# Kernel optimization log

Hardware: AMD Instinct MI355X
Metric: run time of the kernel (lower is better)

Reference implementation:

```python
import jax, jax.numpy as jnp
import numpy as np

T, N, F, H, E = 12, 10000, 32, 64, 320000


def setup_inputs() -> dict:
    key = jax.random.key(0)
    ks = jax.random.split(key, 6)
    x = jax.random.normal(ks[0], (T, N, F), dtype=jnp.float32)
    edge_index = jax.random.randint(ks[1], (2, E), 0, N, dtype=jnp.int64)
    edge_weight = jax.random.uniform(ks[2], (E,), dtype=jnp.float32)
    missing_mask = jnp.ones((T, N, F), dtype=jnp.bool_)
    # GCNConv params (Glorot-ish init); PyG lin: out = x @ W, bias added after aggregation
    W1 = jax.random.normal(ks[3], (F, H), dtype=jnp.float32) * (1.0 / np.sqrt(F))
    b1 = jnp.zeros((H,), dtype=jnp.float32)
    W2 = jax.random.normal(ks[4], (H, F), dtype=jnp.float32) * (1.0 / np.sqrt(H))
    b2 = jnp.zeros((F,), dtype=jnp.float32)
    return dict(x=x, edge_index=edge_index, edge_weight=edge_weight,
                missing_mask=missing_mask, W1=W1, b1=b1, W2=W2, b2=b2)


def _gcn_norm(edge_weight, row, col, n_nodes):
    # PyG gcn_norm with add_self_loops=False: deg from dst, sym normalization
    deg = jax.ops.segment_sum(edge_weight, col, num_segments=n_nodes)
    dinv = jnp.where(deg > 0, 1.0 / jnp.sqrt(jnp.maximum(deg, 1e-12)), 0.0)
    return dinv[row] * edge_weight * dinv[col]


def _gcn_layer(h, row, col, norm, W, b):
    # h: (T, N, Fin) -> (T, N, Fout). Gather at src, weight, scatter-add at dst.
    h = h @ W                                   # (T, N, Fout)
    msg = h[:, row, :] * norm[None, :, None]    # (T, E, Fout)
    out = jnp.zeros((h.shape[0], h.shape[1], h.shape[2]), h.dtype)
    out = out.at[:, col, :].add(msg)
    return out + b


def reference(x, edge_index, edge_weight, missing_mask, W1, b1, W2, b2):
    n_nodes = x.shape[1]
    row, col = edge_index[0], edge_index[1]
    norm = _gcn_norm(edge_weight, row, col, n_nodes)
    h = _gcn_layer(x, row, col, norm, W1, b1)   # layer 0
    h = jax.nn.relu(h)                          # relu between layers
    h = _gcn_layer(h, row, col, norm, W2, b2)   # layer 1 (out_dim = in_dim)
    return jnp.tanh(h)                          # original returns (x, 0); we return x
```

## Files before the change

### kernel.cpp

```cpp
#include <hip/hip_runtime.h>
#include <hip/hip_fp16.h>

#define T_DIM   12
#define N_NODES 10000
#define F_IN    32
#define H_DIM   64
#define NCH     3
#define TC      4
#define CHROW   (TC * F_IN)
#define NGRP    (N_NODES / 16)
#define NTASK   (NCH * NGRP)
#define NROWS   (NCH * N_NODES * TC)
#define MROWS   128

__global__ void zero_kernel(uint4* __restrict__ p, int n16) {
    int i = blockIdx.x * blockDim.x + threadIdx.x;
    if (i < n16) p[i] = make_uint4(0, 0, 0, 0);
}

__global__ void deg_hist_conv_kernel(const int* __restrict__ col,
                                     const float* __restrict__ w,
                                     float* __restrict__ deg,
                                     int* __restrict__ cnt, int E, int eb,
                                     const float* __restrict__ x,
                                     __half* __restrict__ xh) {
    int b = blockIdx.x;
    if (b < eb) {
        int e = b * 256 + threadIdx.x;
        if (e >= E) return;
        int c = col[e];
        atomicAdd(&deg[c], w[e]);
        atomicAdd(&cnt[c], 1);
    } else {
        int task = (b - eb) * 4 + (threadIdx.x >> 6);
        if (task >= NTASK) return;
        int l  = threadIdx.x & 63;
        int ch = task / NGRP;
        int ng = task - ch * NGRP;
        int n  = ng * 16 + (l >> 2);
        int t  = ch * TC + (l & 3);
        const float4* xp = (const float4*)(x + ((size_t)t * N_NODES + n) * F_IN);
        union { uint32_t u[16]; uint4 q[4]; } pk;
#pragma unroll
        for (int i = 0; i < 8; i++) {
            float4 v = xp[i];
            __half2 h0 = __floats2half2_rn(v.x, v.y);
            __half2 h1 = __floats2half2_rn(v.z, v.w);
            pk.u[2 * i]     = *(uint32_t*)&h0;
            pk.u[2 * i + 1] = *(uint32_t*)&h1;
        }
        uint4* dp = (uint4*)(xh + ((size_t)ch * N_NODES * TC + ng * 64 + l) * F_IN);
#pragma unroll
        for (int i = 0; i < 4; i++) dp[i] = pk.q[i];
    }
}

__global__ __launch_bounds__(1024) void scan_kernel(const int* __restrict__ cnt,
                                                    int* __restrict__ rowptr,
                                                    int* __restrict__ cur, int n) {
    __shared__ int part[1024];
    int tid = threadIdx.x;
    const int per = (n + 1023) / 1024;
    int base = tid * per;
    int s = 0;
    for (int i = 0; i < per; i++) {
        int idx = base + i;
        if (idx < n) s += cnt[idx];
    }
    part[tid] = s;
    __syncthreads();
    for (int off = 1; off < 1024; off <<= 1) {
        int v = 0;
        if (tid >= off) v = part[tid - off];
        __syncthreads();
        if (tid >= off) part[tid] += v;
        __syncthreads();
    }
    int run = (tid == 0) ? 0 : part[tid - 1];
    for (int i = 0; i < per; i++) {
        int idx = base + i;
        if (idx < n) { rowptr[idx] = run; cur[idx] = run; run += cnt[idx]; }
    }
    if (tid == 1023) rowptr[n] = part[1023];
}

__global__ void fill_kernel(const int* __restrict__ row,
                            const int* __restrict__ col,
                            const float* __restrict__ w,
                            const float* __restrict__ deg,
                            int* __restrict__ cur,
                            int2* __restrict__ edge_s, int E) {
    int e = blockIdx.x * blockDim.x + threadIdx.x;
    if (e >= E) return;
    int r = row[e];
    int c = col[e];
    float dr = deg[r];
    float dc = deg[c];
    float ir = dr > 0.f ? 1.0f / sqrtf(fmaxf(dr, 1e-12f)) : 0.f;
    float ic = dc > 0.f ? 1.0f / sqrtf(fmaxf(dc, 1e-12f)) : 0.f;
    float nw = ir * w[e] * ic;
    int pos = atomicAdd(&cur[c], 1);
    edge_s[pos] = make_int2(r, __float_as_int(nw));
}

template <bool TANH>
__global__ __launch_bounds__(256) void gather64_kernel(const int* __restrict__ rowptr,
                                                       const int2* __restrict__ edge_s,
                                                       const __half* __restrict__ yh,
                                                       const float* __restrict__ bias,
                                                       float* __restrict__ outp, int n) {
    int c = blockIdx.x * 4 + (threadIdx.x >> 6);
    if (c >= n) return;
    int l    = threadIdx.x & 63;
    int half = l >> 5;
    int l32  = l & 31;

    int beg = rowptr[c], end = rowptr[c + 1];
    const __half* base = yh + 4 * l32;
    const size_t cstep = (size_t)N_NODES * CHROW;

    float4 a0 = {0.f, 0.f, 0.f, 0.f};
    float4 a1 = {0.f, 0.f, 0.f, 0.f};
    float4 a2 = {0.f, 0.f, 0.f, 0.f};

#pragma unroll 4
    for (int e = beg + half; e < end; e += 2) {
        int2 ed = edge_s[e];
        float nw = __int_as_float(ed.y);
        const __half* p = base + (size_t)ed.x * CHROW;
        uint2 u0 = *(const uint2*)(p);
        uint2 u1 = *(const uint2*)(p + cstep);
        uint2 u2 = *(const uint2*)(p + 2 * cstep);
        float2 f00 = __half22float2(*(__half2*)&u0.x), f01 = __half22float2(*(__half2*)&u0.y);
        float2 f10 = __half22float2(*(__half2*)&u1.x), f11 = __half22float2(*(__half2*)&u1.y);
        float2 f20 = __half22float2(*(__half2*)&u2.x), f21 = __half22float2(*(__half2*)&u2.y);
        a0.x = fmaf(f00.x, nw, a0.x); a0.y = fmaf(f00.y, nw, a0.y);
        a0.z = fmaf(f01.x, nw, a0.z); a0.w = fmaf(f01.y, nw, a0.w);
        a1.x = fmaf(f10.x, nw, a1.x); a1.y = fmaf(f10.y, nw, a1.y);
        a1.z = fmaf(f11.x, nw, a1.z); a1.w = fmaf(f11.y, nw, a1.w);
        a2.x = fmaf(f20.x, nw, a2.x); a2.y = fmaf(f20.y, nw, a2.y);
        a2.z = fmaf(f21.x, nw, a2.z); a2.w = fmaf(f21.y, nw, a2.w);
    }

    a0.x += __shfl_xor(a0.x, 32); a0.y += __shfl_xor(a0.y, 32);
    a0.z += __shfl_xor(a0.z, 32); a0.w += __shfl_xor(a0.w, 32);
    a1.x += __shfl_xor(a1.x, 32); a1.y += __shfl_xor(a1.y, 32);
    a1.z += __shfl_xor(a1.z, 32); a1.w += __shfl_xor(a1.w, 32);
    a2.x += __shfl_xor(a2.x, 32); a2.y += __shfl_xor(a2.y, 32);
    a2.z += __shfl_xor(a2.z, 32); a2.w += __shfl_xor(a2.w, 32);

    if (TANH) {
        float4 b4 = *(const float4*)(bias + 4 * (l32 & 7));
        if (half == 0) {
            a0.x = tanhf(a0.x + b4.x); a0.y = tanhf(a0.y + b4.y);
            a0.z = tanhf(a0.z + b4.z); a0.w = tanhf(a0.w + b4.w);
            a1.x = tanhf(a1.x + b4.x); a1.y = tanhf(a1.y + b4.y);
            a1.z = tanhf(a1.z + b4.z); a1.w = tanhf(a1.w + b4.w);
            int t0 = (l32 >> 3);
            float* op0 = outp + ((size_t)t0 * N_NODES + c) * F_IN + 4 * (l32 & 7);
            *(float4*)(op0)                              = a0;
            *(float4*)(op0 + (size_t)TC * N_NODES * F_IN) = a1;
        } else {
            a2.x = tanhf(a2.x + b4.x); a2.y = tanhf(a2.y + b4.y);
            a2.z = tanhf(a2.z + b4.z); a2.w = tanhf(a2.w + b4.w);
            int t2 = 2 * TC + (l32 >> 3);
            float* op2 = outp + ((size_t)t2 * N_NODES + c) * F_IN + 4 * (l32 & 7);
            *(float4*)op2 = a2;
        }
    } else {
        float* op = outp + (size_t)c * CHROW + 4 * l32;
        const size_t ostep = (size_t)N_NODES * CHROW;
        if (half == 0) {
            *(float4*)(op)         = a0;
            *(float4*)(op + ostep) = a1;
        } else {
            *(float4*)(op + 2 * ostep) = a2;
        }
    }
}

__global__ __launch_bounds__(128) void mlp_kernel(const float* __restrict__ aggx,
                                                  const float* __restrict__ W1g,
                                                  const float* __restrict__ b1,
                                                  const float* __restrict__ W2g,
                                                  __half* __restrict__ y2h) {
    __shared__ float W1s[F_IN * H_DIM];
    __shared__ float W2s[H_DIM * F_IN];
    __shared__ float b1s[H_DIM];
    __shared__ float xs[MROWS][F_IN + 1];
    __shared__ float hs[MROWS][H_DIM + 1];

    int tid = threadIdx.x;
    for (int i = tid; i < F_IN * H_DIM; i += 128) { W1s[i] = W1g[i]; W2s[i] = W2g[i]; }
    if (tid < H_DIM) b1s[tid] = b1[tid];

    size_t row0 = (size_t)blockIdx.x * MROWS;
    const float4* src = (const float4*)(aggx + row0 * F_IN);
    for (int i = tid; i < MROWS * (F_IN / 4); i += 128) {
        float4 v = src[i];
        int r = i >> 3, q = (i & 7) * 4;
        xs[r][q + 0] = v.x; xs[r][q + 1] = v.y; xs[r][q + 2] = v.z; xs[r][q + 3] = v.w;
    }
    __syncthreads();

    int rg = tid >> 2;
    int cg = tid & 3;
    int r0 = 4 * rg;

    {
        int c0 = 16 * cg;
        float acc[4][16];
#pragma unroll
        for (int j = 0; j < 16; j++) {
            float b = b1s[c0 + j];
#pragma unroll
            for (int rr = 0; rr < 4; rr++) acc[rr][j] = b;
        }
#pragma unroll 8
        for (int k = 0; k < F_IN; k++) {
            float xr[4];
#pragma unroll
            for (int rr = 0; rr < 4; rr++) xr[rr] = xs[r0 + rr][k];
#pragma unroll
            for (int j = 0; j < 16; j++) {
                float wv = W1s[k * H_DIM + c0 + j];
#pragma unroll
                for (int rr = 0; rr < 4; rr++) acc[rr][j] = fmaf(xr[rr], wv, acc[rr][j]);
            }
        }
#pragma unroll
        for (int rr = 0; rr < 4; rr++)
#pragma unroll
            for (int j = 0; j < 16; j++)
                hs[r0 + rr][c0 + j] = fmaxf(acc[rr][j], 0.f);
    }
    __syncthreads();

    {
        int d0 = 8 * cg;
        float acc[4][8];
#pragma unroll
        for (int rr = 0; rr < 4; rr++)
#pragma unroll
            for (int j = 0; j < 8; j++) acc[rr][j] = 0.f;
#pragma unroll 8
        for (int k = 0; k < H_DIM; k++) {
            float hr[4];
#pragma unroll
            for (int rr = 0; rr < 4; rr++) hr[rr] = hs[r0 + rr][k];
#pragma unroll
            for (int j = 0; j < 8; j++) {
                float wv = W2s[k * F_IN + d0 + j];
#pragma unroll
                for (int rr = 0; rr < 4; rr++) acc[rr][j] = fmaf(hr[rr], wv, acc[rr][j]);
            }
        }
#pragma unroll
        for (int rr = 0; rr < 4; rr++) {
            union { uint32_t u[4]; uint4 q; } pk;
#pragma unroll
            for (int i = 0; i < 4; i++) {
                __half2 hh = __floats2half2_rn(acc[rr][2 * i], acc[rr][2 * i + 1]);
                pk.u[i] = *(uint32_t*)&hh;
            }
            *(uint4*)(y2h + (row0 + r0 + rr) * F_IN + d0) = pk.q;
        }
    }
}

extern "C" void kernel_launch(void* const* d_in, const int* in_sizes, int n_in,
                              void* d_out, int out_size, void* d_ws, size_t ws_size,
                              hipStream_t stream) {
    const float* x  = (const float*)d_in[0];
    const int*   ei = (const int*)d_in[1];
    const float* w  = (const float*)d_in[2];
    const float* W1 = (const float*)d_in[4];
    const float* b1 = (const float*)d_in[5];
    const float* W2 = (const float*)d_in[6];
    const float* b2 = (const float*)d_in[7];
    float* out = (float*)d_out;

    const int E = in_sizes[1] / 2;
    const int* row = ei;
    const int* col = ei + E;

    char* ws = (char*)d_ws;
    size_t off = 0;
    auto alloc = [&](size_t bytes) { void* p = ws + off; off += (bytes + 255) & ~(size_t)255; return p; };
    float*  deg    = (float*) alloc(N_NODES * sizeof(float));
    int*    cnt    = (int*)   alloc(N_NODES * sizeof(int));
    int*    cur    = (int*)   alloc(N_NODES * sizeof(int));
    int*    rowptr = (int*)   alloc((N_NODES + 1) * sizeof(int));
    int2*   edge_s = (int2*)  alloc((size_t)E * sizeof(int2));
    __half* xh     = (__half*)alloc((size_t)NROWS * F_IN * sizeof(__half));
    __half* y2h    = (__half*)alloc((size_t)(NROWS + 64) * F_IN * sizeof(__half));
    float*  aggx   = (float*) alloc((size_t)(NROWS + 64) * F_IN * sizeof(float));

    const int eb = (E + 255) / 256;
    const int cb = (NTASK + 3) / 4;
    const int gb = (N_NODES + 3) / 4;
    const int mb = (NROWS + MROWS - 1) / MROWS;

    const int zn = (int)(((char*)(cnt + N_NODES) - (char*)deg) / 16);
    zero_kernel<<<(zn + 255) / 256, 256, 0, stream>>>((uint4*)deg, zn);
    deg_hist_conv_kernel<<<eb + cb, 256, 0, stream>>>(col, w, deg, cnt, E, eb, x, xh);
    scan_kernel<<<1, 1024, 0, stream>>>(cnt, rowptr, cur, N_NODES);
    fill_kernel<<<eb, 256, 0, stream>>>(row, col, w, deg, cur, edge_s, E);

    gather64_kernel<false><<<gb, 256, 0, stream>>>(rowptr, edge_s, xh, nullptr, aggx, N_NODES);
    mlp_kernel<<<mb, 128, 0, stream>>>(aggx, W1, b1, W2, y2h);

    gather64_kernel<true><<<gb, 256, 0, stream>>>(rowptr, edge_s, y2h, b2, out, N_NODES);
}
```

Measured before the change: 165.8 us.

## Pack degree and count into one 64-bit atomic and precompute dinv

Replaces the separate float degree and int count atomics with a single 64-bit atomic holding a 20-bit fixed-point weight sum in the low bits and the edge count in the high bits. The returned old count gives each edge its slot within its destination, so the fill kernel no longer needs a second atomic on a cursor array. The scan kernel also computes rsqrt of each degree once, so fill reads dinv instead of doing per-edge sqrt and division. In exchange, the degree becomes fixed-point with limited precision and overflow headroom, and the extra per-edge posE buffer costs memory traffic.

Measured after the change: 137.1 us. -17.3%, faster.

```diff
diff --git a/kernel.cpp b/kernel.cpp
--- a/kernel.cpp
+++ b/kernel.cpp
@@ -13,6 +13,10 @@
 #define NROWS   (NCH * N_NODES * TC)
 #define MROWS   128
 
+#define CNT_SHIFT 40
+#define FIX_SCALE 1048576.0f
+#define FIX_MASK  ((1ull << CNT_SHIFT) - 1)
+
 __global__ void zero_kernel(uint4* __restrict__ p, int n16) {
     int i = blockIdx.x * blockDim.x + threadIdx.x;
     if (i < n16) p[i] = make_uint4(0, 0, 0, 0);
@@ -20,8 +24,8 @@
 
 __global__ void deg_hist_conv_kernel(const int* __restrict__ col,
                                      const float* __restrict__ w,
-                                     float* __restrict__ deg,
-                                     int* __restrict__ cnt, int E, int eb,
+                                     unsigned long long* __restrict__ packed,
+                                     unsigned int* __restrict__ posE, int E, int eb,
                                      const float* __restrict__ x,
                                      __half* __restrict__ xh) {
     int b = blockIdx.x;
@@ -29,8 +33,9 @@
         int e = b * 256 + threadIdx.x;
         if (e >= E) return;
         int c = col[e];
-        atomicAdd(&deg[c], w[e]);
-        atomicAdd(&cnt[c], 1);
+        unsigned long long fx = (unsigned long long)(w[e] * FIX_SCALE + 0.5f);
+        unsigned long long old = atomicAdd(&packed[c], (1ull << CNT_SHIFT) | fx);
+        posE[e] = (unsigned int)(old >> CNT_SHIFT);
     } else {
         int task = (b - eb) * 4 + (threadIdx.x >> 6);
         if (task >= NTASK) return;
@@ -55,9 +60,9 @@
     }
 }
 
-__global__ __launch_bounds__(1024) void scan_kernel(const int* __restrict__ cnt,
+__global__ __launch_bounds__(1024) void scan_kernel(const unsigned long long* __restrict__ packed,
                                                     int* __restrict__ rowptr,
-                                                    int* __restrict__ cur, int n) {
+                                                    float* __restrict__ dinv, int n) {
     __shared__ int part[1024];
     int tid = threadIdx.x;
     const int per = (n + 1023) / 1024;
@@ -65,7 +70,12 @@
     int s = 0;
     for (int i = 0; i < per; i++) {
         int idx = base + i;
-        if (idx < n) s += cnt[idx];
+        if (idx < n) {
+            unsigned long long p = packed[idx];
+            s += (int)(p >> CNT_SHIFT);
+            float deg = (float)(p & FIX_MASK) * (1.0f / FIX_SCALE);
+            dinv[idx] = deg > 0.f ? rsqrtf(deg) : 0.f;
+        }
     }
     part[tid] = s;
     __syncthreads();
@@ -79,7 +89,10 @@
     int run = (tid == 0) ? 0 : part[tid - 1];
     for (int i = 0; i < per; i++) {
         int idx = base + i;
-        if (idx < n) { rowptr[idx] = run; cur[idx] = run; run += cnt[idx]; }
+        if (idx < n) {
+            rowptr[idx] = run;
+            run += (int)(packed[idx] >> CNT_SHIFT);
+        }
     }
     if (tid == 1023) rowptr[n] = part[1023];
 }
@@ -87,19 +100,16 @@
 __global__ void fill_kernel(const int* __restrict__ row,
                             const int* __restrict__ col,
                             const float* __restrict__ w,
-                            const float* __restrict__ deg,
-                            int* __restrict__ cur,
+                            const float* __restrict__ dinv,
+                            const int* __restrict__ rowptr,
+                            const unsigned int* __restrict__ posE,
                             int2* __restrict__ edge_s, int E) {
     int e = blockIdx.x * blockDim.x + threadIdx.x;
     if (e >= E) return;
     int r = row[e];
     int c = col[e];
-    float dr = deg[r];
-    float dc = deg[c];
-    float ir = dr > 0.f ? 1.0f / sqrtf(fmaxf(dr, 1e-12f)) : 0.f;
-    float ic = dc > 0.f ? 1.0f / sqrtf(fmaxf(dc, 1e-12f)) : 0.f;
-    float nw = ir * w[e] * ic;
-    int pos = atomicAdd(&cur[c], 1);
+    float nw = dinv[r] * w[e] * dinv[c];
+    int pos = rowptr[c] + (int)posE[e];
     edge_s[pos] = make_int2(r, __float_as_int(nw));
 }
 
@@ -158,7 +168,7 @@
             a1.z = tanhf(a1.z + b4.z); a1.w = tanhf(a1.w + b4.w);
             int t0 = (l32 >> 3);
             float* op0 = outp + ((size_t)t0 * N_NODES + c) * F_IN + 4 * (l32 & 7);
-            *(float4*)(op0)                              = a0;
+            *(float4*)(op0)                               = a0;
             *(float4*)(op0 + (size_t)TC * N_NODES * F_IN) = a1;
         } else {
             a2.x = tanhf(a2.x + b4.x); a2.y = tanhf(a2.y + b4.y);
@@ -287,10 +297,10 @@
     char* ws = (char*)d_ws;
     size_t off = 0;
     auto alloc = [&](size_t bytes) { void* p = ws + off; off += (bytes + 255) & ~(size_t)255; return p; };
-    float*  deg    = (float*) alloc(N_NODES * sizeof(float));
-    int*    cnt    = (int*)   alloc(N_NODES * sizeof(int));
-    int*    cur    = (int*)   alloc(N_NODES * sizeof(int));
+    unsigned long long* packed = (unsigned long long*)alloc(N_NODES * sizeof(unsigned long long));
+    unsigned int* posE   = (unsigned int*)alloc((size_t)E * sizeof(unsigned int));
     int*    rowptr = (int*)   alloc((N_NODES + 1) * sizeof(int));
+    float*  dinv   = (float*) alloc(N_NODES * sizeof(float));
     int2*   edge_s = (int2*)  alloc((size_t)E * sizeof(int2));
     __half* xh     = (__half*)alloc((size_t)NROWS * F_IN * sizeof(__half));
     __half* y2h    = (__half*)alloc((size_t)(NROWS + 64) * F_IN * sizeof(__half));
@@ -301,11 +311,11 @@
     const int gb = (N_NODES + 3) / 4;
     const int mb = (NROWS + MROWS - 1) / MROWS;
 
-    const int zn = (int)(((char*)(cnt + N_NODES) - (char*)deg) / 16);
-    zero_kernel<<<(zn + 255) / 256, 256, 0, stream>>>((uint4*)deg, zn);
-    deg_hist_conv_kernel<<<eb + cb, 256, 0, stream>>>(col, w, deg, cnt, E, eb, x, xh);
-    scan_kernel<<<1, 1024, 0, stream>>>(cnt, rowptr, cur, N_NODES);
-    fill_kernel<<<eb, 256, 0, stream>>>(row, col, w, deg, cur, edge_s, E);
+    const int zn = (N_NODES * 8) / 16;
+    zero_kernel<<<(zn + 255) / 256, 256, 0, stream>>>((uint4*)packed, zn);
+    deg_hist_conv_kernel<<<eb + cb, 256, 0, stream>>>(col, w, packed, posE, E, eb, x, xh);
+    scan_kernel<<<1, 1024, 0, stream>>>(packed, rowptr, dinv, N_NODES);
+    fill_kernel<<<eb, 256, 0, stream>>>(row, col, w, dinv, rowptr, posE, edge_s, E);
 
     gather64_kernel<false><<<gb, 256, 0, stream>>>(rowptr, edge_s, xh, nullptr, aggx, N_NODES);
     mlp_kernel<<<mb, 128, 0, stream>>>(aggx, W1, b1, W2, y2h);
```
